# Optimization experiments

Measured on AMD Instinct MI355X. Metric: run time of the kernel, lower is better.

Reference implementation:

```python
import jax, jax.numpy as jnp
import numpy as np

B, T, M = 4, 1024, 512
H, K, V = 8, 64, 64
EPS = 1e-6


def setup_inputs() -> dict:
    key = jax.random.key(0)
    ks = jax.random.split(key, 8)
    s = 1.0 / np.sqrt(M)
    return {
        "query": jax.random.normal(ks[0], (B, T, M), jnp.float32),
        "key": jax.random.normal(ks[1], (B, T, M), jnp.float32),
        "value": jax.random.normal(ks[2], (B, T, M), jnp.float32),
        "Wq": jax.random.normal(ks[3], (M, H * K), jnp.float32) * s,
        "Wk": jax.random.normal(ks[4], (M, H * K), jnp.float32) * s,
        "Wv": jax.random.normal(ks[5], (M, H * V), jnp.float32) * s,
        # gate linear is zero-initialized in the original (Constant(0.0)); use
        # small random weights so the gate path is exercised numerically.
        "Wg": jax.random.normal(ks[6], (M, H * V), jnp.float32) * (0.02 * s),
        "bg": jnp.zeros((H * V,), jnp.float32),
        "Wo": jax.random.normal(ks[7], (H * V, M), jnp.float32) * (1.0 / np.sqrt(H * V)),
    }


def _phi(x):
    return jax.nn.elu(x) + 1.0


def reference(query, key, value, Wq, Wk, Wv, Wg, bg, Wo):
    # projections -> [B, T, H, d]
    q = (query @ Wq).reshape(B, T, H, K)
    k = (key @ Wk).reshape(B, T, H, K)
    v = (value @ Wv).reshape(B, T, H, V)

    qf = _phi(q)
    kf = _phi(k)

    # multiplicative value gate from the raw value input
    gate = jax.nn.sigmoid((value @ Wg + bg).reshape(B, T, H, V))
    v = v * (2.0 * gate)

    # visualization attention map: qf . kf, causal, row-normalized
    scores = jnp.einsum("bthk,bshk->bhts", qf, kf)  # [B,H,T,T]
    causal = (jnp.arange(T)[None, :] <= jnp.arange(T)[:, None]).astype(scores.dtype)
    scores = scores * causal[None, None]
    att_map = scores / (jnp.sum(scores, axis=-1, keepdims=True) + EPS)

    # causal linear attention via cumulative sums (Tq == Tk so the idx-take
    # in the original is an identity gather)
    kv = jnp.einsum("bthk,bthv->bthkv", kf, v)  # [B,T,H,K,V]
    kv_cum = jnp.cumsum(kv, axis=1)
    k_cum = jnp.cumsum(kf, axis=1)               # [B,T,H,K]

    numer = jnp.einsum("bthk,bthkv->bthv", qf, kv_cum)
    denom = jnp.einsum("bthk,bthk->bth", qf, k_cum) + EPS
    out = (numer / denom[..., None]).reshape(B, T, H * V)
    out = out @ Wo  # [B,T,M]
    return out, att_map
```

## Files before the change

kernel.cpp:

```cpp
#include <hip/hip_runtime.h>
#include <cstdint>

#define TDIM 1024
#define BDIM 4
#define EPSF 1e-6f

#define OFF_KSUM  32768u
#define OFF_KV    65536u
#define FLOAT_BYTES 8650752u
#define UOFF_QP 0u
#define UOFF_KP 2097152u
#define UOFF_VP 4194304u
#define UOFF_NB 6291456u
#define UOFF_WQ 8388608u
#define UOFF_WK 8650752u
#define UOFF_WV 8912896u
#define UOFF_WG 9175040u
#define UOFF_WO 9437184u

typedef short bf16x8 __attribute__((ext_vector_type(8)));
typedef float f32x4  __attribute__((ext_vector_type(4)));
typedef unsigned short ushort_t;

union bfu { int4 i4; unsigned short us[8]; bf16x8 v; };

__device__ __forceinline__ float phi_f(float x)  { return x > 0.f ? x + 1.f : __expf(x); }
__device__ __forceinline__ float sigm_f(float x) { return 1.f / (1.f + __expf(-x)); }
__device__ __forceinline__ unsigned short f2b(float x) {
    union { float f; unsigned u; } v; v.f = x;
    return (unsigned short)((v.u + 0x7FFFu + ((v.u >> 16) & 1u)) >> 16);
}
__device__ __forceinline__ float b2f(unsigned short s) {
    union { unsigned u; float f; } v; v.u = (unsigned)s << 16; return v.f;
}
__device__ __forceinline__ int4 pack8(float4 a, float4 b) {
    bfu u;
    u.us[0] = f2b(a.x); u.us[1] = f2b(a.y); u.us[2] = f2b(a.z); u.us[3] = f2b(a.w);
    u.us[4] = f2b(b.x); u.us[5] = f2b(b.y); u.us[6] = f2b(b.z); u.us[7] = f2b(b.w);
    return u.i4;
}
#define FMA4(ACC, S, V) do { (ACC).x += (S)*(V).x; (ACC).y += (S)*(V).y; \
                             (ACC).z += (S)*(V).z; (ACC).w += (S)*(V).w; } while (0)

__global__ __launch_bounds__(256) void castwt_all(const float* __restrict__ W0,
                                                  const float* __restrict__ W1,
                                                  const float* __restrict__ W2,
                                                  const float* __restrict__ W3,
                                                  const float* __restrict__ W4,
                                                  ushort_t* __restrict__ T0,
                                                  ushort_t* __restrict__ T1,
                                                  ushort_t* __restrict__ T2,
                                                  ushort_t* __restrict__ T3,
                                                  ushort_t* __restrict__ T4) {
    const float* W; ushort_t* Wt;
    switch (blockIdx.z) {
        case 0: W = W0; Wt = T0; break;
        case 1: W = W1; Wt = T1; break;
        case 2: W = W2; Wt = T2; break;
        case 3: W = W3; Wt = T3; break;
        default: W = W4; Wt = T4; break;
    }
    __shared__ unsigned short tile[32][36];
    const int t = threadIdx.x;
    const int r0 = blockIdx.y * 32, c0 = blockIdx.x * 32;
    {
        const int r = t >> 3, c4 = (t & 7) * 4;
        float4 x = *(const float4*)(W + (size_t)(r0 + r) * 512 + c0 + c4);
        tile[c4 + 0][r] = f2b(x.x); tile[c4 + 1][r] = f2b(x.y);
        tile[c4 + 2][r] = f2b(x.z); tile[c4 + 3][r] = f2b(x.w);
    }
    __syncthreads();
    const int c = t >> 3, r4 = (t & 7) * 4;
    ushort4 o;
    o.x = tile[c][r4 + 0]; o.y = tile[c][r4 + 1];
    o.z = tile[c][r4 + 2]; o.w = tile[c][r4 + 3];
    *(ushort4*)(Wt + (size_t)(c0 + c) * 512 + r0 + r4) = o;
}

__global__ __launch_bounds__(256) void proj_k(const float* __restrict__ query,
                                              const float* __restrict__ key_,
                                              const float* __restrict__ value,
                                              const ushort_t* __restrict__ wqt,
                                              const ushort_t* __restrict__ wkt,
                                              const ushort_t* __restrict__ wvt,
                                              const ushort_t* __restrict__ wgt,
                                              const float* __restrict__ bg,
                                              ushort_t* __restrict__ qp,
                                              ushort_t* __restrict__ kp,
                                              ushort_t* __restrict__ vp) {
    __shared__ __align__(16) unsigned short As[2][4096];
    __shared__ __align__(16) unsigned short Bs[2][4096];
    __shared__ __align__(16) unsigned short Bs2[2][2048];
    const int z = blockIdx.z;
    const bool dual = (z >= 2);
    const float* A = (z == 0) ? query : (z == 1) ? key_ : value;
    const ushort_t* B0 = (z == 0) ? wqt : (z == 1) ? wkt : wvt;
    ushort_t* outp = (z == 0) ? qp : (z == 1) ? kp : vp;

    const int tid = threadIdx.x;
    const int row0 = blockIdx.x * 64, n0 = blockIdx.y * 64;
    const int nbase = dual ? (n0 + (z - 2) * 32) : n0;
    const int w = tid >> 6, lane = tid & 63;
    const int cc = tid & 7, rr = tid >> 3;
    const int fm = lane & 15, fq = lane >> 4;
    const int la0 = (cc * 64 + (rr ^ cc)) * 8;
    const int la1 = (cc * 64 + ((rr + 32) ^ cc)) * 8;
    const int lg0 = (cc * 32 + (rr ^ cc)) * 8;

    f32x4 acc[4], acc2[2];
#pragma unroll
    for (int i = 0; i < 4; i++) acc[i] = (f32x4){0.f, 0.f, 0.f, 0.f};
#pragma unroll
    for (int i = 0; i < 2; i++) acc2[i] = (f32x4){0.f, 0.f, 0.f, 0.f};

    const float*    aptr = A   + (size_t)(row0 + rr) * 512 + cc * 8;
    const ushort_t* bptr = B0  + (size_t)(nbase + rr) * 512 + cc * 8;
    const ushort_t* gptr = wgt + (size_t)(nbase + rr) * 512 + cc * 8;

    float4 a0 = *(const float4*)(aptr);
    float4 a1 = *(const float4*)(aptr + 4);
    float4 a2 = *(const float4*)(aptr + 32 * 512);
    float4 a3 = *(const float4*)(aptr + 32 * 512 + 4);
    int4 b0 = *(const int4*)(bptr);
    int4 b1 = {0, 0, 0, 0}, g0 = {0, 0, 0, 0};
    if (dual) g0 = *(const int4*)(gptr);
    else      b1 = *(const int4*)(bptr + 32 * 512);
    *(int4*)&As[0][la0] = pack8(a0, a1);
    *(int4*)&As[0][la1] = pack8(a2, a3);
    *(int4*)&Bs[0][la0] = b0;
    if (dual) *(int4*)&Bs2[0][lg0] = g0;
    else      *(int4*)&Bs[0][la1] = b1;
    __syncthreads();

    for (int kti = 0; kti < 8; kti++) {
        const int buf = kti & 1;
        if (kti < 7) {
            const int off = (kti + 1) * 64;
            a0 = *(const float4*)(aptr + off);
            a1 = *(const float4*)(aptr + off + 4);
            a2 = *(const float4*)(aptr + off + 32 * 512);
            a3 = *(const float4*)(aptr + off + 32 * 512 + 4);
            b0 = *(const int4*)(bptr + off);
            if (dual) g0 = *(const int4*)(gptr + off);
            else      b1 = *(const int4*)(bptr + off + 32 * 512);
        }
        if (dual) {
#pragma unroll
            for (int j = 0; j < 2; j++) {
                const int cu = j * 4 + fq;
                bf16x8 af = *(const bf16x8*)&As[buf][(cu * 64 + ((w * 16 + fm) ^ cu)) * 8];
#pragma unroll
                for (int nb = 0; nb < 2; nb++) {
                    bf16x8 bv = *(const bf16x8*)&Bs[buf][(cu * 64 + ((nb * 16 + fm) ^ cu)) * 8];
                    bf16x8 gv = *(const bf16x8*)&Bs2[buf][(cu * 32 + ((nb * 16 + fm) ^ cu)) * 8];
                    acc[nb]  = __builtin_amdgcn_mfma_f32_16x16x32_bf16(af, bv, acc[nb], 0, 0, 0);
                    acc2[nb] = __builtin_amdgcn_mfma_f32_16x16x32_bf16(af, gv, acc2[nb], 0, 0, 0);
                }
            }
        } else {
#pragma unroll
            for (int j = 0; j < 2; j++) {
                const int cu = j * 4 + fq;
                bf16x8 af = *(const bf16x8*)&As[buf][(cu * 64 + ((w * 16 + fm) ^ cu)) * 8];
#pragma unroll
                for (int nb = 0; nb < 4; nb++) {
                    bf16x8 bv = *(const bf16x8*)&Bs[buf][(cu * 64 + ((nb * 16 + fm) ^ cu)) * 8];
                    acc[nb] = __builtin_amdgcn_mfma_f32_16x16x32_bf16(af, bv, acc[nb], 0, 0, 0);
                }
            }
        }
        if (kti < 7) {
            const int nb_ = buf ^ 1;
            *(int4*)&As[nb_][la0] = pack8(a0, a1);
            *(int4*)&As[nb_][la1] = pack8(a2, a3);
            *(int4*)&Bs[nb_][la0] = b0;
            if (dual) *(int4*)&Bs2[nb_][lg0] = g0;
            else      *(int4*)&Bs[nb_][la1] = b1;
            __syncthreads();
        }
    }

    if (dual) {
#pragma unroll
        for (int nb = 0; nb < 2; nb++) {
            const int col = nbase + nb * 16 + fm;
            const float bb = bg[col];
#pragma unroll
            for (int r = 0; r < 4; r++) {
                const int row = row0 + w * 16 + fq * 4 + r;
                outp[(size_t)row * 512 + col] =
                    f2b(acc[nb][r] * 2.f * sigm_f(acc2[nb][r] + bb));
            }
        }
    } else {
#pragma unroll
        for (int nb = 0; nb < 4; nb++) {
            const int col = n0 + nb * 16 + fm;
#pragma unroll
            for (int r = 0; r < 4; r++) {
                const int row = row0 + w * 16 + fq * 4 + r;
                outp[(size_t)row * 512 + col] = f2b(phi_f(acc[nb][r]));
            }
        }
    }
}

__global__ __launch_bounds__(256) void outproj_k(const ushort_t* __restrict__ A,
                                                 const ushort_t* __restrict__ Bt,
                                                 float* __restrict__ out) {
    __shared__ __align__(16) unsigned short As[2][4096];
    __shared__ __align__(16) unsigned short Bs[2][4096];
    const int tid = threadIdx.x;
    const int row0 = blockIdx.x * 64, n0 = blockIdx.y * 64;
    const int w = tid >> 6, lane = tid & 63;
    const int cc = tid & 7, rr = tid >> 3;
    const int fm = lane & 15, fq = lane >> 4;
    const int la0 = (cc * 64 + (rr ^ cc)) * 8;
    const int la1 = (cc * 64 + ((rr + 32) ^ cc)) * 8;

    f32x4 acc[4];
#pragma unroll
    for (int i = 0; i < 4; i++) acc[i] = (f32x4){0.f, 0.f, 0.f, 0.f};

    const ushort_t* aptr = A  + (size_t)(row0 + rr) * 512 + cc * 8;
    const ushort_t* bptr = Bt + (size_t)(n0 + rr) * 512 + cc * 8;
    int4 ra0 = *(const int4*)(aptr);
    int4 ra1 = *(const int4*)(aptr + 32 * 512);
    int4 rb0 = *(const int4*)(bptr);
    int4 rb1 = *(const int4*)(bptr + 32 * 512);
    *(int4*)&As[0][la0] = ra0; *(int4*)&As[0][la1] = ra1;
    *(int4*)&Bs[0][la0] = rb0; *(int4*)&Bs[0][la1] = rb1;
    __syncthreads();

    for (int kti = 0; kti < 8; kti++) {
        const int buf = kti & 1;
        if (kti < 7) {
            const int off = (kti + 1) * 64;
            ra0 = *(const int4*)(aptr + off);
            ra1 = *(const int4*)(aptr + off + 32 * 512);
            rb0 = *(const int4*)(bptr + off);
            rb1 = *(const int4*)(bptr + off + 32 * 512);
        }
#pragma unroll
        for (int j = 0; j < 2; j++) {
            const int cu = j * 4 + fq;
            bf16x8 af = *(const bf16x8*)&As[buf][(cu * 64 + ((w * 16 + fm) ^ cu)) * 8];
#pragma unroll
            for (int nb = 0; nb < 4; nb++) {
                bf16x8 bv = *(const bf16x8*)&Bs[buf][(cu * 64 + ((nb * 16 + fm) ^ cu)) * 8];
                acc[nb] = __builtin_amdgcn_mfma_f32_16x16x32_bf16(af, bv, acc[nb], 0, 0, 0);
            }
        }
        if (kti < 7) {
            const int nb_ = buf ^ 1;
            *(int4*)&As[nb_][la0] = ra0; *(int4*)&As[nb_][la1] = ra1;
            *(int4*)&Bs[nb_][la0] = rb0; *(int4*)&Bs[nb_][la1] = rb1;
            __syncthreads();
        }
    }
#pragma unroll
    for (int nb = 0; nb < 4; nb++) {
        const int col = n0 + nb * 16 + fm;
#pragma unroll
        for (int r = 0; r < 4; r++) {
            const int row = row0 + w * 16 + fq * 4 + r;
            __builtin_nontemporal_store(acc[nb][r], &out[(size_t)row * 512 + col]);
        }
    }
}

__global__ __launch_bounds__(256) void chunksum_k(const ushort_t* __restrict__ kb,
                                                  const ushort_t* __restrict__ vb,
                                                  float* __restrict__ kv,
                                                  float* __restrict__ ksum) {
    __shared__ __align__(16) float kf_c[64][68];
    __shared__ __align__(16) float vg_c[64][68];
    const int tid = threadIdx.x;
    const int bh = blockIdx.x, c = blockIdx.y;
    const int b = bh >> 3, h = bh & 7;
    const int r = tid >> 2, qq = tid & 3;
    {
        const size_t rowbase = ((size_t)(b * TDIM + c * 64 + r)) * 512 + h * 64 + qq * 16;
        bfu k0, k1, v0, v1;
        k0.i4 = *(const int4*)(kb + rowbase);
        k1.i4 = *(const int4*)(kb + rowbase + 8);
        v0.i4 = *(const int4*)(vb + rowbase);
        v1.i4 = *(const int4*)(vb + rowbase + 8);
#pragma unroll
        for (int j = 0; j < 8; j++) {
            kf_c[r][qq * 16 + j]     = b2f(k0.us[j]);
            kf_c[r][qq * 16 + 8 + j] = b2f(k1.us[j]);
            vg_c[r][qq * 16 + j]     = b2f(v0.us[j]);
            vg_c[r][qq * 16 + 8 + j] = b2f(v1.us[j]);
        }
    }
    __syncthreads();
    const int k0i = (tid >> 4) * 4;
    const int v0i = (tid & 15) * 4;
    float4 a4[4];
#pragma unroll
    for (int i = 0; i < 4; i++) a4[i] = make_float4(0.f, 0.f, 0.f, 0.f);
    for (int t = 0; t < 64; t++) {
        float4 kk4 = *(const float4*)&kf_c[t][k0i];
        float4 vv  = *(const float4*)&vg_c[t][v0i];
        FMA4(a4[0], kk4.x, vv); FMA4(a4[1], kk4.y, vv);
        FMA4(a4[2], kk4.z, vv); FMA4(a4[3], kk4.w, vv);
    }
    const size_t base = (size_t)(bh * 16 + c) * 64;
#pragma unroll
    for (int i = 0; i < 4; i++)
        *(float4*)(kv + (base + k0i + i) * 64 + v0i) = a4[i];
    if (tid < 64) {
        float s = 0.f;
        for (int t = 0; t < 64; t++) s += kf_c[t][tid];
        ksum[base + tid] = s;
    }
}

__global__ __launch_bounds__(256) void fused_k(const ushort_t* __restrict__ qb,
                                               const ushort_t* __restrict__ kb,
                                               const ushort_t* __restrict__ vb,
                                               const float* __restrict__ kvc,
                                               const float* __restrict__ ksum,
                                               ushort_t* __restrict__ nbo,
                                               float* __restrict__ att) {
    extern __shared__ __align__(16) char smem[];
    unsigned short* qs   = (unsigned short*)smem;
    unsigned short* ksb  = qs + 4096;
    unsigned short* vrow = ksb + 8192;
    float* kvf  = (float*)(vrow + 64 * 72);
    float* sc   = kvf + 64 * 68;
    float* kpre = sc + 64 * 68;
    float* ps   = kpre + 64;
    float* inv_s = ps + 256;

    const int tid = threadIdx.x;
    const int bh = blockIdx.x;
    const int yy = (int)blockIdx.y;
    const int diag = (yy < 8) ? (15 - yy) : (yy - 8);
    const int tt0 = diag * 64;
    const int b = bh >> 3, h = bh & 7;
    const int w = tid >> 6, lane = tid & 63;
    const int fm = lane & 15, fq = lane >> 4;
    const int rr = tid >> 3, cc = tid & 7;
    const int la0 = (cc * 64 + (rr ^ cc)) * 8;
    const int la1 = (cc * 64 + ((rr + 32) ^ cc)) * 8;

    const ushort_t* kbase = kb + ((size_t)(b * TDIM + rr)) * 512 + h * 64 + cc * 8;

    {
        const ushort_t* qptr = qb + ((size_t)(b * TDIM + tt0 + rr)) * 512 + h * 64 + cc * 8;
        *(int4*)&qs[la0] = *(const int4*)qptr;
        *(int4*)&qs[la1] = *(const int4*)(qptr + 32 * 512);
        const ushort_t* kptr = kbase + (size_t)tt0 * 512;
        *(int4*)&ksb[la0] = *(const int4*)kptr;
        *(int4*)&ksb[la1] = *(const int4*)(kptr + 32 * 512);
        const int r = tid >> 2, qq = tid & 3;
        const ushort_t* vptr = vb + ((size_t)(b * TDIM + tt0 + r)) * 512 + h * 64 + qq * 16;
        *(int4*)&vrow[r * 72 + qq * 16]     = *(const int4*)vptr;
        *(int4*)&vrow[r * 72 + qq * 16 + 8] = *(const int4*)(vptr + 8);
        float4 a4[4];
#pragma unroll
        for (int u = 0; u < 4; u++) a4[u] = make_float4(0.f, 0.f, 0.f, 0.f);
        for (int c2 = 0; c2 < diag; c2++) {
            const float* p = kvc + (size_t)(bh * 16 + c2) * 4096 + r * 64 + qq * 16;
#pragma unroll
            for (int u = 0; u < 4; u++) {
                float4 x = *(const float4*)(p + 4 * u);
                a4[u].x += x.x; a4[u].y += x.y; a4[u].z += x.z; a4[u].w += x.w;
            }
        }
#pragma unroll
        for (int u = 0; u < 4; u++) *(float4*)&kvf[r * 68 + qq * 16 + 4 * u] = a4[u];
        if (tid < 64) {
            float s = 0.f;
            for (int c2 = 0; c2 < diag; c2++)
                s += ksum[(size_t)(bh * 16 + c2) * 64 + tid];
            kpre[tid] = s;
        }
    }
    __syncthreads();

    f32x4 sa[4];
    {
        int4 rk0 = {0,0,0,0}, rk1 = {0,0,0,0};
        if (diag > 0) {
            rk0 = *(const int4*)(kbase);
            rk1 = *(const int4*)(kbase + 32 * 512);
        }
#pragma unroll
        for (int i = 0; i < 4; i++) sa[i] = (f32x4){0.f, 0.f, 0.f, 0.f};
#pragma unroll
        for (int j = 0; j < 2; j++) {
            const int cu = j * 4 + fq;
            bf16x8 aqf = *(const bf16x8*)&qs[(cu * 64 + ((w * 16 + fm) ^ cu)) * 8];
#pragma unroll
            for (int nb = 0; nb < 4; nb++) {
                bf16x8 bk = *(const bf16x8*)&ksb[(cu * 64 + ((nb * 16 + fm) ^ cu)) * 8];
                sa[nb] = __builtin_amdgcn_mfma_f32_16x16x32_bf16(aqf, bk, sa[nb], 0, 0, 0);
            }
        }
#pragma unroll
        for (int nb = 0; nb < 4; nb++) {
            const int s_l = nb * 16 + fm;
#pragma unroll
            for (int r = 0; r < 4; r++) {
                const int t_l = w * 16 + fq * 4 + r;
                sc[t_l * 68 + s_l] = (s_l <= t_l) ? sa[nb][r] : 0.f;
            }
        }
        if (diag > 0) {
            *(int4*)&ksb[4096 + la0] = rk0;
            *(int4*)&ksb[4096 + la1] = rk1;
        }
    }
    __syncthreads();

    {
        const int rw = tid >> 2, sq = tid & 3;
        float p = 0.f;
#pragma unroll
        for (int s = sq * 16; s < sq * 16 + 16; s++) p += sc[rw * 68 + s];
#pragma unroll
        for (int kd = sq * 16; kd < sq * 16 + 16; kd++) {
            const int cu = kd >> 3;
            p += b2f(qs[(cu * 64 + (rw ^ cu)) * 8 + (kd & 7)]) * kpre[kd];
        }
        ps[rw * 4 + sq] = p;
    }
    __syncthreads();
    {
        const int rw = tid >> 2, sq = tid & 3;
        if (sq == 0) {
            float den = ps[rw * 4] + ps[rw * 4 + 1] + ps[rw * 4 + 2] + ps[rw * 4 + 3];
            inv_s[rw] = 1.f / (den + EPSF);
        }
    }
    __syncthreads();

    {
        f32x4 oa[4];
#pragma unroll
        for (int i = 0; i < 4; i++) oa[i] = (f32x4){0.f, 0.f, 0.f, 0.f};
        bf16x8 aqv[2], apv[2];
#pragma unroll
        for (int j = 0; j < 2; j++) {
            const int cu = j * 4 + fq;
            aqv[j] = *(const bf16x8*)&qs[(cu * 64 + ((w * 16 + fm) ^ cu)) * 8];
            bfu t;
#pragma unroll
            for (int e2 = 0; e2 < 8; e2++) t.us[e2] = f2b(sc[(w * 16 + fm) * 68 + cu * 8 + e2]);
            apv[j] = t.v;
        }
#pragma unroll
        for (int nb = 0; nb < 4; nb++) {
            const int v = nb * 16 + fm;
#pragma unroll
            for (int j = 0; j < 2; j++) {
                const int cu = j * 4 + fq;
                bfu tkv, tv;
#pragma unroll
                for (int e = 0; e < 8; e++) {
                    tkv.us[e] = f2b(kvf[(cu * 8 + e) * 68 + v]);
                    tv.us[e]  = vrow[(cu * 8 + e) * 72 + v];
                }
                oa[nb] = __builtin_amdgcn_mfma_f32_16x16x32_bf16(aqv[j], tkv.v, oa[nb], 0, 0, 0);
                oa[nb] = __builtin_amdgcn_mfma_f32_16x16x32_bf16(apv[j], tv.v, oa[nb], 0, 0, 0);
            }
        }
#pragma unroll
        for (int nb = 0; nb < 4; nb++) {
            const int vcol = nb * 16 + fm;
#pragma unroll
            for (int r = 0; r < 4; r++) {
                const int t_l = w * 16 + fq * 4 + r;
                const float val = oa[nb][r] * inv_s[t_l];
                nbo[((size_t)(b * TDIM + tt0 + t_l)) * 512 + h * 64 + vcol] = f2b(val);
            }
        }
    }

    bf16x8 aq[2];
    float invr[4];
#pragma unroll
    for (int j = 0; j < 2; j++) {
        const int cu = j * 4 + fq;
        aq[j] = *(const bf16x8*)&qs[(cu * 64 + ((w * 16 + fm) ^ cu)) * 8];
    }
#pragma unroll
    for (int r = 0; r < 4; r++) invr[r] = inv_s[w * 16 + fq * 4 + r];

    float* attb = att + (size_t)bh * TDIM * TDIM;
    int4 rk0, rk1;
    for (int st = 0; st < diag; st++) {
        const int bsel = (st + 1) & 1;
        if (st + 1 < diag) {
            const size_t off = (size_t)(st + 1) * 64 * 512;
            rk0 = *(const int4*)(kbase + off);
            rk1 = *(const int4*)(kbase + off + 32 * 512);
        }
        f32x4 pa[4];
#pragma unroll
        for (int i = 0; i < 4; i++) pa[i] = (f32x4){0.f, 0.f, 0.f, 0.f};
#pragma unroll
        for (int j = 0; j < 2; j++) {
            const int cu = j * 4 + fq;
#pragma unroll
            for (int nb = 0; nb < 4; nb++) {
                bf16x8 bk = *(const bf16x8*)&ksb[bsel * 4096 +
                                                 (cu * 64 + ((nb * 16 + fm) ^ cu)) * 8];
                pa[nb] = __builtin_amdgcn_mfma_f32_16x16x32_bf16(aq[j], bk, pa[nb], 0, 0, 0);
            }
        }
        const int s0 = st * 64;
#pragma unroll
        for (int nb = 0; nb < 4; nb++) {
            const int s_g = s0 + nb * 16 + fm;
#pragma unroll
            for (int r = 0; r < 4; r++) {
                const int t_g = tt0 + w * 16 + fq * 4 + r;
                __builtin_nontemporal_store(pa[nb][r] * invr[r],
                                            &attb[(size_t)t_g * TDIM + s_g]);
            }
        }
        if (st + 1 < diag) {
            *(int4*)&ksb[(bsel ^ 1) * 4096 + la0] = rk0;
            *(int4*)&ksb[(bsel ^ 1) * 4096 + la1] = rk1;
            __syncthreads();
        }
    }
#pragma unroll
    for (int nb = 0; nb < 4; nb++) {
        const int s_l = nb * 16 + fm;
#pragma unroll
        for (int r = 0; r < 4; r++) {
            const int t_l = w * 16 + fq * 4 + r;
            const float val = (s_l <= t_l) ? sa[nb][r] * invr[r] : 0.f;
            __builtin_nontemporal_store(val,
                &attb[(size_t)(tt0 + t_l) * TDIM + tt0 + s_l]);
        }
    }
    {
        const f32x4 z = (f32x4){0.f, 0.f, 0.f, 0.f};
        const int r = tid >> 2, qq = tid & 3;
        float* rowp = attb + (size_t)(tt0 + r) * TDIM;
        for (int c0 = (diag + 1) * 64 + qq * 4; c0 < TDIM; c0 += 16)
            __builtin_nontemporal_store(z, (f32x4*)(rowp + c0));
    }
}

extern "C" void kernel_launch(void* const* d_in, const int* in_sizes, int n_in,
                              void* d_out, int out_size, void* d_ws, size_t ws_size,
                              hipStream_t stream) {
    (void)in_sizes; (void)n_in; (void)out_size; (void)ws_size;
    const float* query = (const float*)d_in[0];
    const float* key   = (const float*)d_in[1];
    const float* value = (const float*)d_in[2];
    const float* Wq    = (const float*)d_in[3];
    const float* Wk    = (const float*)d_in[4];
    const float* Wv    = (const float*)d_in[5];
    const float* Wg    = (const float*)d_in[6];
    const float* bg    = (const float*)d_in[7];
    const float* Wo    = (const float*)d_in[8];
    float* out = (float*)d_out;
    float* att = (float*)d_out + 2097152;
    float* ws  = (float*)d_ws;
    float* ksum = ws + OFF_KSUM;
    float* kv   = ws + OFF_KV;
    ushort_t* ub  = (ushort_t*)((char*)d_ws + FLOAT_BYTES);
    ushort_t* qp  = ub + UOFF_QP;
    ushort_t* kp  = ub + UOFF_KP;
    ushort_t* vp  = ub + UOFF_VP;
    ushort_t* nbp = ub + UOFF_NB;
    ushort_t* wqt = ub + UOFF_WQ;
    ushort_t* wkt = ub + UOFF_WK;
    ushort_t* wvt = ub + UOFF_WV;
    ushort_t* wgt = ub + UOFF_WG;
    ushort_t* wot = ub + UOFF_WO;

    dim3 blk(256);
    castwt_all<<<dim3(16, 16, 5), blk, 0, stream>>>(Wq, Wk, Wv, Wg, Wo,
                                                    wqt, wkt, wvt, wgt, wot);
    proj_k<<<dim3(64, 8, 4), blk, 0, stream>>>(query, key, value,
                                               wqt, wkt, wvt, wgt, bg, qp, kp, vp);
    chunksum_k<<<dim3(32, 16), blk, 0, stream>>>(kp, vp, kv, ksum);
    fused_k<<<dim3(32, 16), blk, 70144, stream>>>(qp, kp, vp, kv, ksum, nbp, att);
    outproj_k<<<dim3(64, 8), blk, 0, stream>>>(nbp, wot, out);
}
```

Baseline: 244.5 us.

## Split fused attention-map kernel across two z-blocks and shrink shared memory

```diff
diff --git a/kernel.cpp b/kernel.cpp
--- a/kernel.cpp
+++ b/kernel.cpp
@@ -317,27 +317,31 @@
     }
 }
 
-__global__ __launch_bounds__(256) void fused_k(const ushort_t* __restrict__ qb,
-                                               const ushort_t* __restrict__ kb,
-                                               const ushort_t* __restrict__ vb,
-                                               const float* __restrict__ kvc,
-                                               const float* __restrict__ ksum,
-                                               ushort_t* __restrict__ nbo,
-                                               float* __restrict__ att) {
+__global__ __launch_bounds__(256, 3) void fused_k(const ushort_t* __restrict__ qb,
+                                                  const ushort_t* __restrict__ kb,
+                                                  const ushort_t* __restrict__ vb,
+                                                  const float* __restrict__ kvc,
+                                                  const float* __restrict__ ksum,
+                                                  ushort_t* __restrict__ nbo,
+                                                  float* __restrict__ att) {
     extern __shared__ __align__(16) char smem[];
-    unsigned short* qs   = (unsigned short*)smem;
-    unsigned short* ksb  = qs + 4096;
-    unsigned short* vrow = ksb + 8192;
-    float* kvf  = (float*)(vrow + 64 * 72);
-    float* sc   = kvf + 64 * 68;
-    float* kpre = sc + 64 * 68;
-    float* ps   = kpre + 64;
-    float* inv_s = ps + 256;
+    unsigned short* qs    = (unsigned short*)smem;
+    unsigned short* ksb   = qs + 4096;
+    unsigned short* vrow  = (unsigned short*)(smem + 16384);
+    unsigned short* sc16  = (unsigned short*)(smem + 25600);
+    float* kvf   = (float*)(smem + 34304);
+    float* kpre  = (float*)(smem + 51712);
+    float* ps    = (float*)(smem + 51968);
+    float* inv_s = (float*)(smem + 52992);
 
     const int tid = threadIdx.x;
     const int bh = blockIdx.x;
     const int yy = (int)blockIdx.y;
     const int diag = (yy < 8) ? (15 - yy) : (yy - 8);
+    const bool zlight = (blockIdx.z != 0);
+    const int split = (2 * diag) / 5;
+    const int s_begin = zlight ? split : 0;
+    const int s_end   = zlight ? diag  : split;
     const int tt0 = diag * 64;
     const int b = bh >> 3, h = bh & 7;
     const int w = tid >> 6, lane = tid & 63;
@@ -356,22 +360,24 @@
         *(int4*)&ksb[la0] = *(const int4*)kptr;
         *(int4*)&ksb[la1] = *(const int4*)(kptr + 32 * 512);
         const int r = tid >> 2, qq = tid & 3;
-        const ushort_t* vptr = vb + ((size_t)(b * TDIM + tt0 + r)) * 512 + h * 64 + qq * 16;
-        *(int4*)&vrow[r * 72 + qq * 16]     = *(const int4*)vptr;
-        *(int4*)&vrow[r * 72 + qq * 16 + 8] = *(const int4*)(vptr + 8);
-        float4 a4[4];
-#pragma unroll
-        for (int u = 0; u < 4; u++) a4[u] = make_float4(0.f, 0.f, 0.f, 0.f);
-        for (int c2 = 0; c2 < diag; c2++) {
-            const float* p = kvc + (size_t)(bh * 16 + c2) * 4096 + r * 64 + qq * 16;
-#pragma unroll
-            for (int u = 0; u < 4; u++) {
-                float4 x = *(const float4*)(p + 4 * u);
-                a4[u].x += x.x; a4[u].y += x.y; a4[u].z += x.z; a4[u].w += x.w;
-            }
-        }
-#pragma unroll
-        for (int u = 0; u < 4; u++) *(float4*)&kvf[r * 68 + qq * 16 + 4 * u] = a4[u];
+        if (!zlight) {
+            const ushort_t* vptr = vb + ((size_t)(b * TDIM + tt0 + r)) * 512 + h * 64 + qq * 16;
+            *(int4*)&vrow[r * 72 + qq * 16]     = *(const int4*)vptr;
+            *(int4*)&vrow[r * 72 + qq * 16 + 8] = *(const int4*)(vptr + 8);
+            float4 a4[4];
+#pragma unroll
+            for (int u = 0; u < 4; u++) a4[u] = make_float4(0.f, 0.f, 0.f, 0.f);
+            for (int c2 = 0; c2 < diag; c2++) {
+                const float* p = kvc + (size_t)(bh * 16 + c2) * 4096 + r * 64 + qq * 16;
+#pragma unroll
+                for (int u = 0; u < 4; u++) {
+                    float4 x = *(const float4*)(p + 4 * u);
+                    a4[u].x += x.x; a4[u].y += x.y; a4[u].z += x.z; a4[u].w += x.w;
+                }
+            }
+#pragma unroll
+            for (int u = 0; u < 4; u++) *(float4*)&kvf[r * 68 + qq * 16 + 4 * u] = a4[u];
+        }
         if (tid < 64) {
             float s = 0.f;
             for (int c2 = 0; c2 < diag; c2++)
@@ -382,11 +388,12 @@
     __syncthreads();
 
     f32x4 sa[4];
+    int4 rk0 = {0, 0, 0, 0}, rk1 = {0, 0, 0, 0};
     {
-        int4 rk0 = {0,0,0,0}, rk1 = {0,0,0,0};
-        if (diag > 0) {
-            rk0 = *(const int4*)(kbase);
-            rk1 = *(const int4*)(kbase + 32 * 512);
+        if (s_end > s_begin) {
+            const size_t off = (size_t)s_begin * 64 * 512;
+            rk0 = *(const int4*)(kbase + off);
+            rk1 = *(const int4*)(kbase + off + 32 * 512);
         }
 #pragma unroll
         for (int i = 0; i < 4; i++) sa[i] = (f32x4){0.f, 0.f, 0.f, 0.f};
@@ -406,12 +413,8 @@
 #pragma unroll
             for (int r = 0; r < 4; r++) {
                 const int t_l = w * 16 + fq * 4 + r;
-                sc[t_l * 68 + s_l] = (s_l <= t_l) ? sa[nb][r] : 0.f;
-            }
-        }
-        if (diag > 0) {
-            *(int4*)&ksb[4096 + la0] = rk0;
-            *(int4*)&ksb[4096 + la1] = rk1;
+                sc16[t_l * 68 + s_l] = (s_l <= t_l) ? f2b(sa[nb][r]) : (unsigned short)0;
+            }
         }
     }
     __syncthreads();
@@ -420,7 +423,7 @@
         const int rw = tid >> 2, sq = tid & 3;
         float p = 0.f;
 #pragma unroll
-        for (int s = sq * 16; s < sq * 16 + 16; s++) p += sc[rw * 68 + s];
+        for (int s = sq * 16; s < sq * 16 + 16; s++) p += b2f(sc16[rw * 68 + s]);
 #pragma unroll
         for (int kd = sq * 16; kd < sq * 16 + 16; kd++) {
             const int cu = kd >> 3;
@@ -438,7 +441,12 @@
     }
     __syncthreads();
 
-    {
+    float invr[4];
+#pragma unroll
+    for (int r = 0; r < 4; r++) invr[r] = inv_s[w * 16 + fq * 4 + r];
+    float* attb = att + (size_t)bh * TDIM * TDIM;
+
+    if (!zlight) {
         f32x4 oa[4];
 #pragma unroll
         for (int i = 0; i < 4; i++) oa[i] = (f32x4){0.f, 0.f, 0.f, 0.f};
@@ -449,7 +457,7 @@
             aqv[j] = *(const bf16x8*)&qs[(cu * 64 + ((w * 16 + fm) ^ cu)) * 8];
             bfu t;
 #pragma unroll
-            for (int e2 = 0; e2 < 8; e2++) t.us[e2] = f2b(sc[(w * 16 + fm) * 68 + cu * 8 + e2]);
+            for (int e2 = 0; e2 < 8; e2++) t.us[e2] = sc16[(w * 16 + fm) * 68 + cu * 8 + e2];
             apv[j] = t.v;
         }
 #pragma unroll
@@ -478,74 +486,73 @@
                 nbo[((size_t)(b * TDIM + tt0 + t_l)) * 512 + h * 64 + vcol] = f2b(val);
             }
         }
-    }
-
-    bf16x8 aq[2];
-    float invr[4];
-#pragma unroll
-    for (int j = 0; j < 2; j++) {
-        const int cu = j * 4 + fq;
-        aq[j] = *(const bf16x8*)&qs[(cu * 64 + ((w * 16 + fm) ^ cu)) * 8];
-    }
-#pragma unroll
-    for (int r = 0; r < 4; r++) invr[r] = inv_s[w * 16 + fq * 4 + r];
-
-    float* attb = att + (size_t)bh * TDIM * TDIM;
-    int4 rk0, rk1;
-    for (int st = 0; st < diag; st++) {
-        const int bsel = (st + 1) & 1;
-        if (st + 1 < diag) {
-            const size_t off = (size_t)(st + 1) * 64 * 512;
-            rk0 = *(const int4*)(kbase + off);
-            rk1 = *(const int4*)(kbase + off + 32 * 512);
-        }
-        f32x4 pa[4];
-#pragma unroll
-        for (int i = 0; i < 4; i++) pa[i] = (f32x4){0.f, 0.f, 0.f, 0.f};
-#pragma unroll
-        for (int j = 0; j < 2; j++) {
-            const int cu = j * 4 + fq;
-#pragma unroll
-            for (int nb = 0; nb < 4; nb++) {
-                bf16x8 bk = *(const bf16x8*)&ksb[bsel * 4096 +
-                                                 (cu * 64 + ((nb * 16 + fm) ^ cu)) * 8];
-                pa[nb] = __builtin_amdgcn_mfma_f32_16x16x32_bf16(aq[j], bk, pa[nb], 0, 0, 0);
-            }
-        }
-        const int s0 = st * 64;
+    } else {
 #pragma unroll
         for (int nb = 0; nb < 4; nb++) {
-            const int s_g = s0 + nb * 16 + fm;
+            const int s_l = nb * 16 + fm;
 #pragma unroll
             for (int r = 0; r < 4; r++) {
-                const int t_g = tt0 + w * 16 + fq * 4 + r;
-                __builtin_nontemporal_store(pa[nb][r] * invr[r],
-                                            &attb[(size_t)t_g * TDIM + s_g]);
-            }
-        }
-        if (st + 1 < diag) {
-            *(int4*)&ksb[(bsel ^ 1) * 4096 + la0] = rk0;
-            *(int4*)&ksb[(bsel ^ 1) * 4096 + la1] = rk1;
-            __syncthreads();
-        }
-    }
-#pragma unroll
-    for (int nb = 0; nb < 4; nb++) {
-        const int s_l = nb * 16 + fm;
-#pragma unroll
-        for (int r = 0; r < 4; r++) {
-            const int t_l = w * 16 + fq * 4 + r;
-            const float val = (s_l <= t_l) ? sa[nb][r] * invr[r] : 0.f;
-            __builtin_nontemporal_store(val,
-                &attb[(size_t)(tt0 + t_l) * TDIM + tt0 + s_l]);
-        }
-    }
-    {
+                const int t_l = w * 16 + fq * 4 + r;
+                const float val = (s_l <= t_l) ? sa[nb][r] * invr[r] : 0.f;
+                __builtin_nontemporal_store(val,
+                    &attb[(size_t)(tt0 + t_l) * TDIM + tt0 + s_l]);
+            }
+        }
         const f32x4 z = (f32x4){0.f, 0.f, 0.f, 0.f};
         const int r = tid >> 2, qq = tid & 3;
         float* rowp = attb + (size_t)(tt0 + r) * TDIM;
         for (int c0 = (diag + 1) * 64 + qq * 4; c0 < TDIM; c0 += 16)
             __builtin_nontemporal_store(z, (f32x4*)(rowp + c0));
+    }
+
+    if (s_end > s_begin) {
+        bf16x8 aq[2];
+#pragma unroll
+        for (int j = 0; j < 2; j++) {
+            const int cu = j * 4 + fq;
+            aq[j] = *(const bf16x8*)&qs[(cu * 64 + ((w * 16 + fm) ^ cu)) * 8];
+        }
+        __syncthreads();
+        *(int4*)&ksb[4096 + la0] = rk0;
+        *(int4*)&ksb[4096 + la1] = rk1;
+        __syncthreads();
+        int bufsel = 1;
+        for (int st = s_begin; st < s_end; ++st, bufsel ^= 1) {
+            if (st + 1 < s_end) {
+                const size_t off = (size_t)(st + 1) * 64 * 512;
+                rk0 = *(const int4*)(kbase + off);
+                rk1 = *(const int4*)(kbase + off + 32 * 512);
+            }
+            f32x4 pa[4];
+#pragma unroll
+            for (int i = 0; i < 4; i++) pa[i] = (f32x4){0.f, 0.f, 0.f, 0.f};
+#pragma unroll
+            for (int j = 0; j < 2; j++) {
+                const int cu = j * 4 + fq;
+#pragma unroll
+                for (int nb = 0; nb < 4; nb++) {
+                    bf16x8 bk = *(const bf16x8*)&ksb[bufsel * 4096 +
+                                                     (cu * 64 + ((nb * 16 + fm) ^ cu)) * 8];
+                    pa[nb] = __builtin_amdgcn_mfma_f32_16x16x32_bf16(aq[j], bk, pa[nb], 0, 0, 0);
+                }
+            }
+            const int s0 = st * 64;
+#pragma unroll
+            for (int nb = 0; nb < 4; nb++) {
+                const int s_g = s0 + nb * 16 + fm;
+#pragma unroll
+                for (int r = 0; r < 4; r++) {
+                    const int t_g = tt0 + w * 16 + fq * 4 + r;
+                    __builtin_nontemporal_store(pa[nb][r] * invr[r],
+                                                &attb[(size_t)t_g * TDIM + s_g]);
+                }
+            }
+            if (st + 1 < s_end) {
+                *(int4*)&ksb[(bufsel ^ 1) * 4096 + la0] = rk0;
+                *(int4*)&ksb[(bufsel ^ 1) * 4096 + la1] = rk1;
+                __syncthreads();
+            }
+        }
     }
 }
 
@@ -584,6 +591,6 @@
     proj_k<<<dim3(64, 8, 4), blk, 0, stream>>>(query, key, value,
                                                wqt, wkt, wvt, wgt, bg, qp, kp, vp);
     chunksum_k<<<dim3(32, 16), blk, 0, stream>>>(kp, vp, kv, ksum);
-    fused_k<<<dim3(32, 16), blk, 70144, stream>>>(qp, kp, vp, kv, ksum, nbp, att);
+    fused_k<<<dim3(32, 16, 2), blk, 53248, stream>>>(qp, kp, vp, kv, ksum, nbp, att);
     outproj_k<<<dim3(64, 8), blk, 0, stream>>>(nbp, wot, out);
 }
```

Measured after the change: 246.7 us. Within noise of the previous version (+0.9%).
